# Kernel tuning notes

Hardware: AMD Instinct MI355X
Metric: run time of the kernel (lower is better)

Reference implementation:

```python
import jax, jax.numpy as jnp
import numpy as np

D = 1024
H = 16
HD = D // H
S = 2048
B = 2
HID = D * 7 // 2  # 3584


def _linear_params(key, din, dout):
    kw, kb = jax.random.split(key)
    bound = 1.0 / np.sqrt(din)
    W = jax.random.uniform(kw, (dout, din), jnp.float32, -bound, bound)
    b = jax.random.uniform(kb, (dout,), jnp.float32, -bound, bound)
    return W, b


def setup_inputs() -> dict:
    key = jax.random.key(0)
    ks = jax.random.split(key, 9)
    x = jax.random.normal(ks[0], (B, S, D), jnp.float32)
    pos_emb = 0.02 * jax.random.normal(ks[1], (1, S, D), jnp.float32)
    q_w, q_b = _linear_params(ks[2], D, D)
    k_w, k_b = _linear_params(ks[3], D, D)
    v_w, v_b = _linear_params(ks[4], D, D)
    o_w, o_b = _linear_params(ks[5], D, D)
    in_w, in_b = _linear_params(ks[6], D, HID)
    gate_w, gate_b = _linear_params(ks[7], D, HID)
    out_w, out_b = _linear_params(ks[8], HID, D)
    norm1_w = jnp.ones((D,), jnp.float32)
    norm2_w = jnp.ones((D,), jnp.float32)
    return dict(x=x, pos_emb=pos_emb, norm1_w=norm1_w, norm2_w=norm2_w,
                q_w=q_w, q_b=q_b, k_w=k_w, k_b=k_b, v_w=v_w, v_b=v_b,
                o_w=o_w, o_b=o_b, in_w=in_w, in_b=in_b,
                gate_w=gate_w, gate_b=gate_b, out_w=out_w, out_b=out_b)


def _rmsnorm(x, w, eps=1e-6):
    return x * jax.lax.rsqrt(jnp.mean(x * x, axis=-1, keepdims=True) + eps) * w


def _attn(x, q_w, q_b, k_w, k_b, v_w, v_b, o_w, o_b):
    b, s, _ = x.shape
    q = (x @ q_w.T + q_b).reshape(b, s, H, HD)
    k = (x @ k_w.T + k_b).reshape(b, s, H, HD)
    v = (x @ v_w.T + v_b).reshape(b, s, H, HD)
    scores = jnp.einsum('bqhd,bkhd->bhqk', q, k) / jnp.sqrt(jnp.float32(HD))
    causal = jnp.tril(jnp.ones((s, s), bool))  # True = keep
    scores = jnp.where(causal, scores, -jnp.inf)
    p = jax.nn.softmax(scores, axis=-1)
    o = jnp.einsum('bhqk,bkhd->bqhd', p, v).reshape(b, s, D)
    return o @ o_w.T + o_b


def _mlp(x, in_w, in_b, gate_w, gate_b, out_w, out_b):
    gate = jax.nn.silu(x @ gate_w.T + gate_b)
    h = gate * (x @ in_w.T + in_b)
    return h @ out_w.T + out_b


def reference(x, pos_emb, norm1_w, norm2_w, q_w, q_b, k_w, k_b, v_w, v_b,
              o_w, o_b, in_w, in_b, gate_w, gate_b, out_w, out_b):
    x = x + pos_emb
    x = x + _attn(_rmsnorm(x, norm1_w), q_w, q_b, k_w, k_b, v_w, v_b, o_w, o_b)
    x = x + _mlp(_rmsnorm(x, norm2_w), in_w, in_b, gate_w, gate_b, out_w, out_b)
    return x
```

## Files before the change

kernel.cpp:

```cpp
#include <hip/hip_runtime.h>

typedef __attribute__((ext_vector_type(4))) float f32x4;
typedef __attribute__((ext_vector_type(8))) short bf16x8;
typedef unsigned short u16;

constexpr int kB = 2, kS = 2048, kD = 1024, kH = 16, kHD = 64, kHID = 3584;
constexpr int kN = kB * kS;

__device__ __forceinline__ u16 f2bf(float f) {
  unsigned u = __float_as_uint(f);
  u = (u + 0x7FFFu + ((u >> 16) & 1u)) >> 16;
  return (u16)u;
}
__device__ __forceinline__ float bf2f(u16 v) {
  return __uint_as_float((unsigned)v << 16);
}

__device__ __forceinline__ float rowmax16(float v) {
  int t;
  t = __builtin_amdgcn_update_dpp(0, __float_as_int(v), 0x121, 0xf, 0xf, true);
  v = fmaxf(v, __int_as_float(t));
  t = __builtin_amdgcn_update_dpp(0, __float_as_int(v), 0x122, 0xf, 0xf, true);
  v = fmaxf(v, __int_as_float(t));
  t = __builtin_amdgcn_update_dpp(0, __float_as_int(v), 0x124, 0xf, 0xf, true);
  v = fmaxf(v, __int_as_float(t));
  t = __builtin_amdgcn_update_dpp(0, __float_as_int(v), 0x128, 0xf, 0xf, true);
  v = fmaxf(v, __int_as_float(t));
  return v;
}

#define AS1(p) ((const __attribute__((address_space(1))) void*)(p))
#define AS3(p) ((__attribute__((address_space(3))) void*)(p))

__global__ __launch_bounds__(256) void k_prep(
    const float* __restrict__ x, const float* __restrict__ pos,
    const float* __restrict__ w, float* __restrict__ xr, u16* __restrict__ xn) {
  const int n = blockIdx.x, t = threadIdx.x, s = n & (kS - 1);
  float4 a = ((const float4*)(x + (size_t)n * kD))[t];
  float4 p = ((const float4*)(pos + (size_t)s * kD))[t];
  a.x += p.x; a.y += p.y; a.z += p.z; a.w += p.w;
  ((float4*)(xr + (size_t)n * kD))[t] = a;
  float ss = a.x*a.x + a.y*a.y + a.z*a.z + a.w*a.w;
#pragma unroll
  for (int off = 1; off < 64; off <<= 1) ss += __shfl_xor(ss, off);
  __shared__ float red[4];
  if ((t & 63) == 0) red[t >> 6] = ss;
  __syncthreads();
  float rs = rsqrtf((red[0] + red[1] + red[2] + red[3]) * (1.0f / kD) + 1e-6f);
  float4 wv = ((const float4*)w)[t];
  ushort4 o;
  o.x = f2bf(a.x * rs * wv.x); o.y = f2bf(a.y * rs * wv.y);
  o.z = f2bf(a.z * rs * wv.z); o.w = f2bf(a.w * rs * wv.w);
  ((ushort4*)(xn + (size_t)n * kD))[t] = o;
}

__global__ __launch_bounds__(256) void k_rms2(
    const float* __restrict__ xin, const float* __restrict__ w, u16* __restrict__ xn) {
  const int n = blockIdx.x, t = threadIdx.x;
  float4 a = ((const float4*)(xin + (size_t)n * kD))[t];
  float ss = a.x*a.x + a.y*a.y + a.z*a.z + a.w*a.w;
#pragma unroll
  for (int off = 1; off < 64; off <<= 1) ss += __shfl_xor(ss, off);
  __shared__ float red[4];
  if ((t & 63) == 0) red[t >> 6] = ss;
  __syncthreads();
  float rs = rsqrtf((red[0] + red[1] + red[2] + red[3]) * (1.0f / kD) + 1e-6f);
  float4 wv = ((const float4*)w)[t];
  ushort4 o;
  o.x = f2bf(a.x * rs * wv.x); o.y = f2bf(a.y * rs * wv.y);
  o.z = f2bf(a.z * rs * wv.z); o.w = f2bf(a.w * rs * wv.w);
  ((ushort4*)(xn + (size_t)n * kD))[t] = o;
}

__device__ __forceinline__ void cvt4(const float* __restrict__ s, u16* __restrict__ d, int j) {
  float4 v = ((const float4*)s)[j];
  ushort4 o;
  o.x = f2bf(v.x); o.y = f2bf(v.y); o.z = f2bf(v.z); o.w = f2bf(v.w);
  ((ushort4*)d)[j] = o;
}

__global__ __launch_bounds__(256) void k_wprep(
    const float* __restrict__ q_w, const float* __restrict__ k_w,
    const float* __restrict__ v_w, const float* __restrict__ o_w,
    const float* __restrict__ in_w, const float* __restrict__ gate_w,
    const float* __restrict__ out_w,
    const float* __restrict__ q_b, const float* __restrict__ k_b,
    const float* __restrict__ v_b,
    u16* __restrict__ W, float* __restrict__ bqkv) {
  const int i = blockIdx.x * 256 + threadIdx.x;
  if (i < 262144)       cvt4(q_w,    W + 0,        i);
  else if (i < 524288)  cvt4(k_w,    W + 1048576,  i - 262144);
  else if (i < 786432)  cvt4(v_w,    W + 2097152,  i - 524288);
  else if (i < 1048576) cvt4(o_w,    W + 3145728,  i - 786432);
  else if (i < 1966080) cvt4(in_w,   W + 4194304,  i - 1048576);
  else if (i < 2883584) cvt4(gate_w, W + 7864320,  i - 1966080);
  else if (i < 3801088) cvt4(out_w,  W + 11534336, i - 2883584);
  else {
    const int j = i - 3801088;
    const float* src = j < 256 ? q_b : (j < 512 ? k_b : v_b);
    ((float4*)bqkv)[j] = ((const float4*)src)[j & 255];
  }
}

template <int MODE, int BM>
__global__ __launch_bounds__(256) void k_gemm(
    const u16* __restrict__ A, const u16* __restrict__ Bw,
    const float* __restrict__ bias, const void* extra,
    void* outp, int M, int N, int K, int nR, int nC) {
  constexpr int ASEG = BM / 16;
  constexpr int NSEG = ASEG + 8;
  constexpr int WROWS = BM / 2;
  constexpr int MF = BM / 32;
  __shared__ __align__(16) u16 As[2][BM * 32];
  __shared__ __align__(16) u16 Bs[2][128 * 32];
  const int tid = threadIdx.x, lane = tid & 63, wv_ = tid >> 6;
  const int lr = lane & 15, lg = lane >> 4;
  const int xcd = blockIdx.x & 7, idx = blockIdx.x >> 3;
  const int xrr = xcd >> 2, xcc = xcd & 3;
  const int r_ = idx % nR, c_ = idx / nR;
  const int brow = (xrr * nR + r_) * BM, bcol = (xcc * nC + c_) * 128;
  const int wr = wv_ >> 1, wc = wv_ & 1;

  const f32x4 zz = {0.f, 0.f, 0.f, 0.f};
  f32x4 acc[MF][4];
#pragma unroll
  for (int m = 0; m < MF; m++)
#pragma unroll
    for (int n = 0; n < 4; n++) acc[m][n] = zz;

  auto stage = [&](int kt, int buf) {
#pragma unroll
    for (int i = 0; i < NSEG / 4; ++i) {
      const int seg = i * 4 + wv_;
      const int rsub = (seg < ASEG) ? seg : seg - ASEG;
      const int row = rsub * 16 + (lane >> 2), cs = lane & 3;
      if (seg < ASEG) {
        __builtin_amdgcn_global_load_lds(AS1(A + (size_t)(brow + row) * K + kt + cs * 8),
                                         AS3((char*)&As[buf][0] + (size_t)seg * 1024), 16, 0, 0);
      } else {
        __builtin_amdgcn_global_load_lds(AS1(Bw + (size_t)(bcol + row) * K + kt + cs * 8),
                                         AS3((char*)&Bs[buf][0] + (size_t)(seg - ASEG) * 1024), 16, 0, 0);
      }
    }
  };

  stage(0, 0);
  __syncthreads();
  for (int kt = 0; kt < K; kt += 32) {
    const int cur = (kt >> 5) & 1;
    if (kt + 32 < K) stage(kt + 32, cur ^ 1);
    bf16x8 af[MF], bfr[4];
#pragma unroll
    for (int m = 0; m < MF; m++) af[m] = *(const bf16x8*)&As[cur][(wr * WROWS + m * 16 + lr) * 32 + lg * 8];
#pragma unroll
    for (int n = 0; n < 4; n++) bfr[n] = *(const bf16x8*)&Bs[cur][(wc * 64 + n * 16 + lr) * 32 + lg * 8];
#pragma unroll
    for (int m = 0; m < MF; m++)
#pragma unroll
      for (int n = 0; n < 4; n++)
        acc[m][n] = __builtin_amdgcn_mfma_f32_16x16x32_bf16(af[m], bfr[n], acc[m][n], 0, 0, 0);
    __syncthreads();
  }

#pragma unroll
  for (int m = 0; m < MF; m++) {
    const int row0 = brow + wr * WROWS + m * 16 + lg * 4;
#pragma unroll
    for (int n = 0; n < 4; n++) {
      const int col = bcol + wc * 64 + n * 16 + lr;
      const float bv = bias[col];
#pragma unroll
      for (int r = 0; r < 4; r++) {
        const size_t idx2 = (size_t)(row0 + r) * N + col;
        float v = acc[m][n][r] + bv;
        if (MODE == 0) {
          ((u16*)outp)[idx2] = f2bf(v);
        } else {
          ((float*)outp)[idx2] = v + ((const float*)extra)[idx2];
        }
      }
    }
  }
}

__global__ __launch_bounds__(256, 2) void k_mlp(
    const u16* __restrict__ A, const u16* __restrict__ Bi, const u16* __restrict__ Bg,
    const float* __restrict__ bias_i, const float* __restrict__ bias_g,
    u16* __restrict__ outp, int M, int N, int K) {
  __shared__ __align__(16) u16 AsT[2][128 * 32];
  __shared__ __align__(16) u16 BiT[2][128 * 32];
  __shared__ __align__(16) u16 BgT[2][128 * 32];
  const int tid = threadIdx.x, lane = tid & 63, wv_ = tid >> 6;
  const int lr = lane & 15, lg = lane >> 4;
  const int xcd = blockIdx.x & 7, idx = blockIdx.x >> 3;
  const int xrr = xcd >> 2, xcc = xcd & 3;
  const int r_ = idx & 15, c_ = idx >> 4;
  const int brow = (xrr * 16 + r_) * 128, bcol = (xcc * 7 + c_) * 128;
  const int wr = wv_ >> 1, wc = wv_ & 1;

  const f32x4 zz = {0.f, 0.f, 0.f, 0.f};
  f32x4 accI[4][4], accG[4][4];
#pragma unroll
  for (int m = 0; m < 4; m++)
#pragma unroll
    for (int n = 0; n < 4; n++) { accI[m][n] = zz; accG[m][n] = zz; }

  auto stage = [&](int kt, int buf) {
#pragma unroll
    for (int i = 0; i < 6; ++i) {
      const int seg = i * 4 + wv_;
      const int rsub = seg & 7;
      const int row = rsub * 16 + (lane >> 2), cs = lane & 3;
      const u16* src = (i < 2) ? A : (i < 4 ? Bi : Bg);
      char* dst = (i < 2) ? (char*)&AsT[buf][0] : (i < 4 ? (char*)&BiT[buf][0] : (char*)&BgT[buf][0]);
      __builtin_amdgcn_global_load_lds(
          AS1(src + (size_t)((i < 2 ? brow : bcol) + row) * K + kt + cs * 8),
          AS3(dst + (size_t)rsub * 1024), 16, 0, 0);
    }
  };

  stage(0, 0);
  __syncthreads();
  for (int kt = 0; kt < K; kt += 32) {
    const int cur = (kt >> 5) & 1;
    if (kt + 32 < K) stage(kt + 32, cur ^ 1);
    bf16x8 af[4], bfi[4], bfg[4];
#pragma unroll
    for (int m = 0; m < 4; m++) af[m] = *(const bf16x8*)&AsT[cur][(wr * 64 + m * 16 + lr) * 32 + lg * 8];
#pragma unroll
    for (int n = 0; n < 4; n++) {
      bfi[n] = *(const bf16x8*)&BiT[cur][(wc * 64 + n * 16 + lr) * 32 + lg * 8];
      bfg[n] = *(const bf16x8*)&BgT[cur][(wc * 64 + n * 16 + lr) * 32 + lg * 8];
    }
#pragma unroll
    for (int m = 0; m < 4; m++)
#pragma unroll
      for (int n = 0; n < 4; n++) {
        accI[m][n] = __builtin_amdgcn_mfma_f32_16x16x32_bf16(af[m], bfi[n], accI[m][n], 0, 0, 0);
        accG[m][n] = __builtin_amdgcn_mfma_f32_16x16x32_bf16(af[m], bfg[n], accG[m][n], 0, 0, 0);
      }
    __syncthreads();
  }

#pragma unroll
  for (int m = 0; m < 4; m++) {
    const int row0 = brow + wr * 64 + m * 16 + lg * 4;
#pragma unroll
    for (int n = 0; n < 4; n++) {
      const int col = bcol + wc * 64 + n * 16 + lr;
      const float bi = bias_i[col], bg = bias_g[col];
#pragma unroll
      for (int r = 0; r < 4; r++) {
        const float vi = accI[m][n][r] + bi;
        const float vg = accG[m][n][r] + bg;
        const float g = vg / (1.0f + __expf(-vg));
        outp[(size_t)(row0 + r) * N + col] = f2bf(g * vi);
      }
    }
  }
}

__global__ __launch_bounds__(512) void k_attn(
    const u16* __restrict__ qkv, u16* __restrict__ attn_o) {
  __shared__ __align__(16) u16 Ks[2][64 * 64];
  __shared__ __align__(16) u16 Vt[2][64 * 64];
  __shared__ __align__(16) u16 Pl[8][16 * 64];

  const int tid = threadIdx.x, lane = tid & 63, w = tid >> 6;
  const int g = w >> 2, wi = w & 3;
  const int lr = lane & 15, lg = lane >> 4;
  const int bid = blockIdx.x;
  const int half = bid >> 8, rr = bid & 255;
  const int praw = rr & 15;
  const int p = half ? 15 - praw : praw;
  const int bh = (rr >> 4) | (half << 4);
  const int b = bh >> 4, h = bh & 15;
  const int qb = g == 0 ? 31 - p : p;
  const size_t base = (size_t)b * kS;
  const f32x4 zz = {0.f, 0.f, 0.f, 0.f};
  bf16x8 vones;
#pragma unroll
  for (int j = 0; j < 8; j++) vones[j] = (short)0x3F80;

  bf16x8 qf[2];
#pragma unroll
  for (int ks = 0; ks < 2; ks++)
    qf[ks] = *(const bf16x8*)&qkv[(base + qb * 64 + wi * 16 + lr) * 3072 + h * 64 + ks * 32 + lg * 8];

  f32x4 oacc[4], lacc = zz;
  float mrow[4];
#pragma unroll
  for (int nb = 0; nb < 4; nb++) oacc[nb] = zz;
#pragma unroll
  for (int r = 0; r < 4; r++) mrow[r] = -1e30f;

  const int kvloc = (w << 3) + (lane >> 3);
  const int kchv = ((lane & 7) ^ (lane >> 3)) * 8;
  auto issueK = [&](int t, int buf) {
    __builtin_amdgcn_global_load_lds(
        AS1(qkv + (base + t * 64 + kvloc) * 3072 + 1024 + h * 64 + kchv),
        AS3((char*)&Ks[buf][0] + w * 1024 + (size_t)lane * 16), 16, 0, 0);
  };
  const int srow = tid >> 3, dc = (tid & 7) * 8;
  int4 vr;
  auto issueV = [&](int t) {
    vr = *(const int4*)&qkv[(base + t * 64 + srow) * 3072 + 2048 + h * 64 + dc];
  };
  auto commitV = [&](int buf) {
    char* vb = (char*)&Vt[buf][0];
    const u16* ve = (const u16*)&vr;
#pragma unroll
    for (int j = 0; j < 8; j++) {
      const int d = dc + j;
      *(u16*)(vb + ((d * 128 + srow * 2) ^ ((d & 7) << 4))) = ve[j];
    }
  };

  auto compute = [&](int t, int buf) {
    const char* kbuf = (const char*)&Ks[buf][0];
    const char* vbuf = (const char*)&Vt[buf][0];
    const bool masked = (t == qb);
    f32x4 sc[4];
#pragma unroll
    for (int hn = 0; hn < 4; hn++) sc[hn] = zz;
#pragma unroll
    for (int hn = 0; hn < 4; hn++) {
      const int krow = hn * 16 + lr;
#pragma unroll
      for (int ks = 0; ks < 2; ks++) {
        const int bo = (krow * 128 + (ks * 32 + lg * 8) * 2) ^ ((krow & 7) << 4);
        bf16x8 kf = *(const bf16x8*)(kbuf + bo);
        sc[hn] = __builtin_amdgcn_mfma_f32_16x16x32_bf16(qf[ks], kf, sc[hn], 0, 0, 0);
      }
    }
    float alpha[4];
#pragma unroll
    for (int r = 0; r < 4; r++) {
      const int qa = qb * 64 + wi * 16 + lg * 4 + r;
      float s0 = sc[0][r] * 0.125f, s1 = sc[1][r] * 0.125f;
      float s2 = sc[2][r] * 0.125f, s3 = sc[3][r] * 0.125f;
      if (masked) {
        if (t * 64 + lr > qa) s0 = -1e30f;
        if (t * 64 + 16 + lr > qa) s1 = -1e30f;
        if (t * 64 + 32 + lr > qa) s2 = -1e30f;
        if (t * 64 + 48 + lr > qa) s3 = -1e30f;
      }
      float mx = rowmax16(fmaxf(fmaxf(s0, s1), fmaxf(s2, s3)));
      const float mnew = fmaxf(mrow[r], mx);
      alpha[r] = __expf(mrow[r] - mnew);
      mrow[r] = mnew;
      sc[0][r] = __expf(s0 - mnew); sc[1][r] = __expf(s1 - mnew);
      sc[2][r] = __expf(s2 - mnew); sc[3][r] = __expf(s3 - mnew);
    }
#pragma unroll
    for (int nb = 0; nb < 4; nb++)
#pragma unroll
      for (int r = 0; r < 4; r++) oacc[nb][r] *= alpha[r];
#pragma unroll
    for (int r = 0; r < 4; r++) lacc[r] *= alpha[r];
    char* pw = (char*)&Pl[w][0];
#pragma unroll
    for (int hn = 0; hn < 4; hn++)
#pragma unroll
      for (int r = 0; r < 4; r++) {
        const int prow = lg * 4 + r, pcol = hn * 16 + lr;
        *(u16*)(pw + ((prow * 128 + pcol * 2) ^ ((prow & 7) << 4))) = f2bf(sc[hn][r]);
      }
    bf16x8 pf[2];
#pragma unroll
    for (int ks = 0; ks < 2; ks++)
      pf[ks] = *(const bf16x8*)((const char*)pw + ((lr * 128 + (ks * 32 + lg * 8) * 2) ^ ((lr & 7) << 4)));
#pragma unroll
    for (int nb = 0; nb < 4; nb++) {
      const int vrow = nb * 16 + lr;
#pragma unroll
      for (int ks = 0; ks < 2; ks++) {
        const int bo = (vrow * 128 + (ks * 32 + lg * 8) * 2) ^ ((vrow & 7) << 4);
        bf16x8 vf = *(const bf16x8*)(vbuf + bo);
        oacc[nb] = __builtin_amdgcn_mfma_f32_16x16x32_bf16(pf[ks], vf, oacc[nb], 0, 0, 0);
      }
    }
#pragma unroll
    for (int ks = 0; ks < 2; ks++)
      lacc = __builtin_amdgcn_mfma_f32_16x16x32_bf16(pf[ks], vones, lacc, 0, 0, 0);
  };

  const int nt = 32 - p;
  issueV(0);
  issueK(0, 0);
  commitV(0);
  __syncthreads();
  for (int t = 0; t < nt; ++t) {
    const bool hn = (t + 1 < nt);
    const int buf = t & 1;
    if (hn) { issueV(t + 1); issueK(t + 1, buf ^ 1); }
    if (g == 0 || t <= p) compute(t, buf);
    if (hn) commitV(buf ^ 1);
    __syncthreads();
  }

#pragma unroll
  for (int nb = 0; nb < 4; nb++)
#pragma unroll
    for (int r = 0; r < 4; r++) {
      const int q = qb * 64 + wi * 16 + lg * 4 + r;
      attn_o[(base + q) * kD + h * 64 + nb * 16 + lr] = f2bf(oacc[nb][r] / lacc[r]);
    }
}

constexpr size_t OFF_XR   = 0;
constexpr size_t OFF_XN1  = OFF_XR  + (size_t)kN * kD * 4;
constexpr size_t OFF_XN2  = OFF_XN1 + (size_t)kN * kD * 2;
constexpr size_t OFF_W    = OFF_XN2 + (size_t)kN * kD * 2;
constexpr size_t OFF_BQKV = OFF_W + 15204352ull * 2;
constexpr size_t OFF_ACT  = OFF_BQKV + 3072 * 4;

extern "C" void kernel_launch(void* const* d_in, const int* in_sizes, int n_in,
                              void* d_out, int out_size, void* d_ws, size_t ws_size,
                              hipStream_t stream) {
  const float* x     = (const float*)d_in[0];
  const float* pos   = (const float*)d_in[1];
  const float* n1w   = (const float*)d_in[2];
  const float* n2w   = (const float*)d_in[3];
  const float* q_w   = (const float*)d_in[4];
  const float* q_b   = (const float*)d_in[5];
  const float* k_w   = (const float*)d_in[6];
  const float* k_b   = (const float*)d_in[7];
  const float* v_w   = (const float*)d_in[8];
  const float* v_b   = (const float*)d_in[9];
  const float* o_w   = (const float*)d_in[10];
  const float* o_b   = (const float*)d_in[11];
  const float* in_w  = (const float*)d_in[12];
  const float* in_b  = (const float*)d_in[13];
  const float* gate_w= (const float*)d_in[14];
  const float* gate_b= (const float*)d_in[15];
  const float* out_w = (const float*)d_in[16];
  const float* out_b = (const float*)d_in[17];
  float* outf = (float*)d_out;
  char* ws = (char*)d_ws;

  float* xr   = (float*)(ws + OFF_XR);
  u16*   xn1  = (u16*)(ws + OFF_XN1);
  u16*   xn2  = (u16*)(ws + OFF_XN2);
  u16*   W    = (u16*)(ws + OFF_W);
  float* bqkv = (float*)(ws + OFF_BQKV);
  u16*   qkv  = (u16*)(ws + OFF_ACT);
  u16*   attn_o = (u16*)(ws + OFF_ACT + (size_t)kN * 3072 * 2);
  u16*   hb     = (u16*)(ws + OFF_ACT);

  u16* Wq   = W + 0;
  u16* Wo   = W + 3145728;
  u16* Win  = W + 4194304;
  u16* Wg   = W + 7864320;
  u16* Wout = W + 11534336;

  k_prep<<<kN, 256, 0, stream>>>(x, pos, n1w, xr, xn1);
  k_wprep<<<14851, 256, 0, stream>>>(q_w, k_w, v_w, o_w, in_w, gate_w, out_w,
                                     q_b, k_b, v_b, W, bqkv);

  k_gemm<0, 128><<<768, 256, 0, stream>>>(xn1, Wq, bqkv, nullptr, qkv, kN, 3072, kD, 16, 6);

  k_attn<<<512, 512, 0, stream>>>(qkv, attn_o);

  k_gemm<1, 64><<<512, 256, 0, stream>>>(attn_o, Wo, o_b, xr, outf, kN, kD, kD, 32, 2);

  k_rms2<<<kN, 256, 0, stream>>>(outf, n2w, xn2);

  k_mlp<<<896, 256, 0, stream>>>(xn2, Win, Wg, in_b, gate_b, hb, kN, kHID, kD);

  k_gemm<1, 64><<<512, 256, 0, stream>>>(hb, Wout, out_b, outf, outf, kN, kD, kHID, 32, 2);
}
```

Baseline: 430.2 us.

## Merge prep kernels, add BK=64 output GEMM, lazy softmax rescale in attention

Folds the activation prep and weight conversion into a single launch to cut a kernel boundary. Adds a GEMM variant that stages K-tiles of 64 instead of 32 for the two residual-add GEMMs, halving loop iterations and barriers at the cost of more LDS. In attention, skips the running-max update and rescale of the output accumulators unless some row's max grows by more than 8, trading exact max tracking for fewer exps and multiplies, with some risk of fp32 overflow headroom loss.

```diff
diff --git a/kernel.cpp b/kernel.cpp
--- a/kernel.cpp
+++ b/kernel.cpp
@@ -32,14 +32,62 @@
 #define AS1(p) ((const __attribute__((address_space(1))) void*)(p))
 #define AS3(p) ((__attribute__((address_space(3))) void*)(p))
 
-__global__ __launch_bounds__(256) void k_prep(
+__device__ __forceinline__ void cvt4(const float* __restrict__ s, u16* __restrict__ d, int j) {
+  float4 v = ((const float4*)s)[j];
+  ushort4 o;
+  o.x = f2bf(v.x); o.y = f2bf(v.y); o.z = f2bf(v.z); o.w = f2bf(v.w);
+  ((ushort4*)d)[j] = o;
+}
+
+__global__ __launch_bounds__(256) void k_prepw(
     const float* __restrict__ x, const float* __restrict__ pos,
-    const float* __restrict__ w, float* __restrict__ xr, u16* __restrict__ xn) {
-  const int n = blockIdx.x, t = threadIdx.x, s = n & (kS - 1);
-  float4 a = ((const float4*)(x + (size_t)n * kD))[t];
-  float4 p = ((const float4*)(pos + (size_t)s * kD))[t];
-  a.x += p.x; a.y += p.y; a.z += p.z; a.w += p.w;
-  ((float4*)(xr + (size_t)n * kD))[t] = a;
+    const float* __restrict__ n1w, float* __restrict__ xr, u16* __restrict__ xn,
+    const float* __restrict__ q_w, const float* __restrict__ k_w,
+    const float* __restrict__ v_w, const float* __restrict__ o_w,
+    const float* __restrict__ in_w, const float* __restrict__ gate_w,
+    const float* __restrict__ out_w,
+    const float* __restrict__ q_b, const float* __restrict__ k_b,
+    const float* __restrict__ v_b,
+    u16* __restrict__ W, float* __restrict__ bqkv) {
+  __shared__ float red[4];
+  if (blockIdx.x < (unsigned)kN) {
+    const int n = blockIdx.x, t = threadIdx.x, s = n & (kS - 1);
+    float4 a = ((const float4*)(x + (size_t)n * kD))[t];
+    float4 p = ((const float4*)(pos + (size_t)s * kD))[t];
+    a.x += p.x; a.y += p.y; a.z += p.z; a.w += p.w;
+    ((float4*)(xr + (size_t)n * kD))[t] = a;
+    float ss = a.x*a.x + a.y*a.y + a.z*a.z + a.w*a.w;
+#pragma unroll
+    for (int off = 1; off < 64; off <<= 1) ss += __shfl_xor(ss, off);
+    if ((t & 63) == 0) red[t >> 6] = ss;
+    __syncthreads();
+    float rs = rsqrtf((red[0] + red[1] + red[2] + red[3]) * (1.0f / kD) + 1e-6f);
+    float4 wv = ((const float4*)n1w)[t];
+    ushort4 o;
+    o.x = f2bf(a.x * rs * wv.x); o.y = f2bf(a.y * rs * wv.y);
+    o.z = f2bf(a.z * rs * wv.z); o.w = f2bf(a.w * rs * wv.w);
+    ((ushort4*)(xn + (size_t)n * kD))[t] = o;
+  } else {
+    const int i = (blockIdx.x - kN) * 256 + threadIdx.x;
+    if (i < 262144)       cvt4(q_w,    W + 0,        i);
+    else if (i < 524288)  cvt4(k_w,    W + 1048576,  i - 262144);
+    else if (i < 786432)  cvt4(v_w,    W + 2097152,  i - 524288);
+    else if (i < 1048576) cvt4(o_w,    W + 3145728,  i - 786432);
+    else if (i < 1966080) cvt4(in_w,   W + 4194304,  i - 1048576);
+    else if (i < 2883584) cvt4(gate_w, W + 7864320,  i - 1966080);
+    else if (i < 3801088) cvt4(out_w,  W + 11534336, i - 2883584);
+    else {
+      const int j = i - 3801088;
+      const float* src = j < 256 ? q_b : (j < 512 ? k_b : v_b);
+      ((float4*)bqkv)[j] = ((const float4*)src)[j & 255];
+    }
+  }
+}
+
+__global__ __launch_bounds__(256) void k_rms2(
+    const float* __restrict__ xin, const float* __restrict__ w, u16* __restrict__ xn) {
+  const int n = blockIdx.x, t = threadIdx.x;
+  float4 a = ((const float4*)(xin + (size_t)n * kD))[t];
   float ss = a.x*a.x + a.y*a.y + a.z*a.z + a.w*a.w;
 #pragma unroll
   for (int off = 1; off < 64; off <<= 1) ss += __shfl_xor(ss, off);
@@ -52,54 +100,6 @@
   o.x = f2bf(a.x * rs * wv.x); o.y = f2bf(a.y * rs * wv.y);
   o.z = f2bf(a.z * rs * wv.z); o.w = f2bf(a.w * rs * wv.w);
   ((ushort4*)(xn + (size_t)n * kD))[t] = o;
-}
-
-__global__ __launch_bounds__(256) void k_rms2(
-    const float* __restrict__ xin, const float* __restrict__ w, u16* __restrict__ xn) {
-  const int n = blockIdx.x, t = threadIdx.x;
-  float4 a = ((const float4*)(xin + (size_t)n * kD))[t];
-  float ss = a.x*a.x + a.y*a.y + a.z*a.z + a.w*a.w;
-#pragma unroll
-  for (int off = 1; off < 64; off <<= 1) ss += __shfl_xor(ss, off);
-  __shared__ float red[4];
-  if ((t & 63) == 0) red[t >> 6] = ss;
-  __syncthreads();
-  float rs = rsqrtf((red[0] + red[1] + red[2] + red[3]) * (1.0f / kD) + 1e-6f);
-  float4 wv = ((const float4*)w)[t];
-  ushort4 o;
-  o.x = f2bf(a.x * rs * wv.x); o.y = f2bf(a.y * rs * wv.y);
-  o.z = f2bf(a.z * rs * wv.z); o.w = f2bf(a.w * rs * wv.w);
-  ((ushort4*)(xn + (size_t)n * kD))[t] = o;
-}
-
-__device__ __forceinline__ void cvt4(const float* __restrict__ s, u16* __restrict__ d, int j) {
-  float4 v = ((const float4*)s)[j];
-  ushort4 o;
-  o.x = f2bf(v.x); o.y = f2bf(v.y); o.z = f2bf(v.z); o.w = f2bf(v.w);
-  ((ushort4*)d)[j] = o;
-}
-
-__global__ __launch_bounds__(256) void k_wprep(
-    const float* __restrict__ q_w, const float* __restrict__ k_w,
-    const float* __restrict__ v_w, const float* __restrict__ o_w,
-    const float* __restrict__ in_w, const float* __restrict__ gate_w,
-    const float* __restrict__ out_w,
-    const float* __restrict__ q_b, const float* __restrict__ k_b,
-    const float* __restrict__ v_b,
-    u16* __restrict__ W, float* __restrict__ bqkv) {
-  const int i = blockIdx.x * 256 + threadIdx.x;
-  if (i < 262144)       cvt4(q_w,    W + 0,        i);
-  else if (i < 524288)  cvt4(k_w,    W + 1048576,  i - 262144);
-  else if (i < 786432)  cvt4(v_w,    W + 2097152,  i - 524288);
-  else if (i < 1048576) cvt4(o_w,    W + 3145728,  i - 786432);
-  else if (i < 1966080) cvt4(in_w,   W + 4194304,  i - 1048576);
-  else if (i < 2883584) cvt4(gate_w, W + 7864320,  i - 1966080);
-  else if (i < 3801088) cvt4(out_w,  W + 11534336, i - 2883584);
-  else {
-    const int j = i - 3801088;
-    const float* src = j < 256 ? q_b : (j < 512 ? k_b : v_b);
-    ((float4*)bqkv)[j] = ((const float4*)src)[j & 255];
-  }
 }
 
 template <int MODE, int BM>
@@ -183,6 +183,93 @@
   }
 }
 
+template <int MODE>
+__global__ __launch_bounds__(256) void k_gemm64(
+    const u16* __restrict__ A, const u16* __restrict__ Bw,
+    const float* __restrict__ bias, const void* extra,
+    void* outp, int M, int N, int K, int nR, int nC) {
+  __shared__ __align__(16) u16 As[2][64 * 64];
+  __shared__ __align__(16) u16 Bs[2][128 * 64];
+  const int tid = threadIdx.x, lane = tid & 63, wv_ = tid >> 6;
+  const int lr = lane & 15, lg = lane >> 4;
+  const int xcd = blockIdx.x & 7, idx = blockIdx.x >> 3;
+  const int xrr = xcd >> 2, xcc = xcd & 3;
+  const int r_ = idx % nR, c_ = idx / nR;
+  const int brow = (xrr * nR + r_) * 64, bcol = (xcc * nC + c_) * 128;
+  const int wr = wv_ >> 1, wc = wv_ & 1;
+
+  const f32x4 zz = {0.f, 0.f, 0.f, 0.f};
+  f32x4 acc[2][4];
+#pragma unroll
+  for (int m = 0; m < 2; m++)
+#pragma unroll
+    for (int n = 0; n < 4; n++) acc[m][n] = zz;
+
+  const int lrow = lane >> 3;
+  const int lch = ((lane & 7) ^ lrow) * 8;
+  auto stage = [&](int kt, int buf) {
+#pragma unroll
+    for (int i = 0; i < 6; ++i) {
+      const int seg = i * 4 + wv_;
+      const int rsub = (seg < 8) ? seg : seg - 8;
+      const int row = rsub * 8 + lrow;
+      if (seg < 8) {
+        __builtin_amdgcn_global_load_lds(AS1(A + (size_t)(brow + row) * K + kt + lch),
+                                         AS3((char*)&As[buf][0] + (size_t)seg * 1024), 16, 0, 0);
+      } else {
+        __builtin_amdgcn_global_load_lds(AS1(Bw + (size_t)(bcol + row) * K + kt + lch),
+                                         AS3((char*)&Bs[buf][0] + (size_t)(seg - 8) * 1024), 16, 0, 0);
+      }
+    }
+  };
+
+  stage(0, 0);
+  __syncthreads();
+  for (int kt = 0; kt < K; kt += 64) {
+    const int cur = (kt >> 6) & 1;
+    if (kt + 64 < K) stage(kt + 64, cur ^ 1);
+    bf16x8 af[2][2];
+#pragma unroll
+    for (int m = 0; m < 2; m++)
+#pragma unroll
+      for (int ks = 0; ks < 2; ks++) {
+        const int row = wr * 32 + m * 16 + lr;
+        const int bo = (row * 128 + (ks * 32 + lg * 8) * 2) ^ ((row & 7) << 4);
+        af[m][ks] = *(const bf16x8*)((const char*)&As[cur][0] + bo);
+      }
+#pragma unroll
+    for (int n = 0; n < 4; n++) {
+      const int row = wc * 64 + n * 16 + lr;
+      const int bo0 = (row * 128 + (lg * 8) * 2) ^ ((row & 7) << 4);
+      const int bo1 = (row * 128 + (32 + lg * 8) * 2) ^ ((row & 7) << 4);
+      bf16x8 b0 = *(const bf16x8*)((const char*)&Bs[cur][0] + bo0);
+      bf16x8 b1 = *(const bf16x8*)((const char*)&Bs[cur][0] + bo1);
+#pragma unroll
+      for (int m = 0; m < 2; m++) {
+        acc[m][n] = __builtin_amdgcn_mfma_f32_16x16x32_bf16(af[m][0], b0, acc[m][n], 0, 0, 0);
+        acc[m][n] = __builtin_amdgcn_mfma_f32_16x16x32_bf16(af[m][1], b1, acc[m][n], 0, 0, 0);
+      }
+    }
+    __syncthreads();
+  }
+
+#pragma unroll
+  for (int m = 0; m < 2; m++) {
+    const int row0 = brow + wr * 32 + m * 16 + lg * 4;
+#pragma unroll
+    for (int n = 0; n < 4; n++) {
+      const int col = bcol + wc * 64 + n * 16 + lr;
+      const float bv = bias[col];
+#pragma unroll
+      for (int r = 0; r < 4; r++) {
+        const size_t idx2 = (size_t)(row0 + r) * N + col;
+        float v = acc[m][n][r] + bv;
+        ((float*)outp)[idx2] = v + ((const float*)extra)[idx2];
+      }
+    }
+  }
+}
+
 __global__ __launch_bounds__(256, 2) void k_mlp(
     const u16* __restrict__ A, const u16* __restrict__ Bi, const u16* __restrict__ Bg,
     const float* __restrict__ bias_i, const float* __restrict__ bias_g,
@@ -333,7 +420,8 @@
         sc[hn] = __builtin_amdgcn_mfma_f32_16x16x32_bf16(qf[ks], kf, sc[hn], 0, 0, 0);
       }
     }
-    float alpha[4];
+    float nm[4];
+    bool needv = false;
 #pragma unroll
     for (int r = 0; r < 4; r++) {
       const int qa = qb * 64 + wi * 16 + lg * 4 + r;
@@ -345,19 +433,29 @@
         if (t * 64 + 32 + lr > qa) s2 = -1e30f;
         if (t * 64 + 48 + lr > qa) s3 = -1e30f;
       }
-      float mx = rowmax16(fmaxf(fmaxf(s0, s1), fmaxf(s2, s3)));
-      const float mnew = fmaxf(mrow[r], mx);
-      alpha[r] = __expf(mrow[r] - mnew);
-      mrow[r] = mnew;
-      sc[0][r] = __expf(s0 - mnew); sc[1][r] = __expf(s1 - mnew);
-      sc[2][r] = __expf(s2 - mnew); sc[3][r] = __expf(s3 - mnew);
-    }
-#pragma unroll
-    for (int nb = 0; nb < 4; nb++)
-#pragma unroll
-      for (int r = 0; r < 4; r++) oacc[nb][r] *= alpha[r];
-#pragma unroll
-    for (int r = 0; r < 4; r++) lacc[r] *= alpha[r];
+      sc[0][r] = s0; sc[1][r] = s1; sc[2][r] = s2; sc[3][r] = s3;
+      nm[r] = rowmax16(fmaxf(fmaxf(s0, s1), fmaxf(s2, s3)));
+      needv |= (nm[r] > mrow[r] + 8.0f);
+    }
+    if (__any(needv)) {
+      float alpha[4];
+#pragma unroll
+      for (int r = 0; r < 4; r++) {
+        const float mnew = fmaxf(mrow[r], nm[r]);
+        alpha[r] = __expf(mrow[r] - mnew);
+        mrow[r] = mnew;
+      }
+#pragma unroll
+      for (int nb = 0; nb < 4; nb++)
+#pragma unroll
+        for (int r = 0; r < 4; r++) oacc[nb][r] *= alpha[r];
+#pragma unroll
+      for (int r = 0; r < 4; r++) lacc[r] *= alpha[r];
+    }
+#pragma unroll
+    for (int hn = 0; hn < 4; hn++)
+#pragma unroll
+      for (int r = 0; r < 4; r++) sc[hn][r] = __expf(sc[hn][r] - mrow[r]);
     char* pw = (char*)&Pl[w][0];
 #pragma unroll
     for (int hn = 0; hn < 4; hn++)
@@ -454,19 +552,19 @@
   u16* Wg   = W + 7864320;
   u16* Wout = W + 11534336;
 
-  k_prep<<<kN, 256, 0, stream>>>(x, pos, n1w, xr, xn1);
-  k_wprep<<<14851, 256, 0, stream>>>(q_w, k_w, v_w, o_w, in_w, gate_w, out_w,
-                                     q_b, k_b, v_b, W, bqkv);
+  k_prepw<<<kN + 14851, 256, 0, stream>>>(x, pos, n1w, xr, xn1,
+                                          q_w, k_w, v_w, o_w, in_w, gate_w, out_w,
+                                          q_b, k_b, v_b, W, bqkv);
 
   k_gemm<0, 128><<<768, 256, 0, stream>>>(xn1, Wq, bqkv, nullptr, qkv, kN, 3072, kD, 16, 6);
 
   k_attn<<<512, 512, 0, stream>>>(qkv, attn_o);
 
-  k_gemm<1, 64><<<512, 256, 0, stream>>>(attn_o, Wo, o_b, xr, outf, kN, kD, kD, 32, 2);
+  k_gemm64<1><<<512, 256, 0, stream>>>(attn_o, Wo, o_b, xr, outf, kN, kD, kD, 32, 2);
 
   k_rms2<<<kN, 256, 0, stream>>>(outf, n2w, xn2);
 
   k_mlp<<<896, 256, 0, stream>>>(xn2, Win, Wg, in_b, gate_b, hb, kN, kHID, kD);
 
-  k_gemm<1, 64><<<512, 256, 0, stream>>>(hb, Wout, out_b, outf, outf, kN, kD, kHID, 32, 2);
-}
+  k_gemm64<1><<<512, 256, 0, stream>>>(hb, Wout, out_b, outf, outf, kN, kD, kHID, 32, 2);
+}
```

After: 410.6 us. -4.6%, faster.
